# Kernel tuning notes

Measured on AMD Instinct MI355X. Metric: run time of the kernel, lower is better.

Reference implementation:

```python
import jax, jax.numpy as jnp
import numpy as np

NUM_SCALES = 3
LAMBDA_0 = 1.0
MU_0 = 1.0
KAPPA_LAMBDA = 0.5
KAPPA_MU = 0.5
BASE_WEIGHT = 1.0
GRADIENT_SCALING = 0.1


def tgradient(f, axis):
    """torch.gradient semantics: central diff interior, one-sided at edges (spacing=1)."""
    n = f.shape[axis]
    def sl(a, b):
        idx = [slice(None)] * f.ndim
        idx[axis] = slice(a, b)
        return f[tuple(idx)]
    interior = (sl(2, n) - sl(0, n - 2)) * 0.5
    first = sl(1, 2) - sl(0, 1)
    last = sl(n - 1, n) - sl(n - 2, n - 1)
    return jnp.concatenate([first, interior, last], axis=axis)


def resize1d_linear(x, axis, out_size):
    """1D linear resize along `axis` with align_corners=True."""
    in_size = x.shape[axis]
    if out_size == in_size:
        return x
    denom = max(out_size - 1, 1)
    coords = jnp.arange(out_size, dtype=jnp.float32) * ((in_size - 1) / denom)
    i0 = jnp.floor(coords).astype(jnp.int32)
    i1 = jnp.minimum(i0 + 1, in_size - 1)
    w = (coords - i0.astype(jnp.float32)).astype(x.dtype)
    shape = [1] * x.ndim
    shape[axis] = out_size
    w = w.reshape(shape)
    x0 = jnp.take(x, i0, axis=axis)
    x1 = jnp.take(x, i1, axis=axis)
    return x0 * (1 - w) + x1 * w


def trilinear_downsample(x, scale):
    # F.interpolate(..., scale_factor=1/scale, mode='trilinear', align_corners=True,
    # recompute_scale_factor=True): out_size = floor(in_size / scale); separable linear.
    for axis in (2, 3, 4):
        out_size = int(np.floor(x.shape[axis] / scale))
        x = resize1d_linear(x, axis, out_size)
    return x


def elasticity_loss(deformation_field, image):
    total_loss = jnp.float32(0.0)
    for i in range(NUM_SCALES):
        scale = 2 ** i
        deform = trilinear_downsample(deformation_field, scale)
        img = trilinear_downsample(image, scale)
        u, v, w = deform[:, 0], deform[:, 1], deform[:, 2]  # each (B, X, Y, Z)
        du_dx, du_dy, du_dz = tgradient(u, 1), tgradient(u, 2), tgradient(u, 3)
        dv_dx, dv_dy, dv_dz = tgradient(v, 1), tgradient(v, 2), tgradient(v, 3)
        dw_dx, dw_dy, dw_dz = tgradient(w, 1), tgradient(w, 2), tgradient(w, 3)
        E_xx, E_yy, E_zz = du_dx, dv_dy, dw_dz
        E_xy = 0.5 * (du_dy + dv_dx)
        E_xz = 0.5 * (du_dz + dw_dx)
        E_yz = 0.5 * (dv_dz + dw_dy)
        trace_E = E_xx + E_yy + E_zz
        ic = img[:, 0]  # (B, X, Y, Z)
        gx, gy, gz = tgradient(ic, 1), tgradient(ic, 2), tgradient(ic, 3)
        image_gradient = jnp.sqrt(gx * gx + gy * gy + gz * gz)
        adaptive_lambda = LAMBDA_0 + KAPPA_LAMBDA * image_gradient
        adaptive_mu = MU_0 + KAPPA_MU * image_gradient
        elastic_energy = (0.5 * adaptive_lambda * trace_E ** 2
                          + adaptive_mu * (E_xx ** 2 + E_yy ** 2 + E_zz ** 2
                                           + 2.0 * (E_xy ** 2 + E_xz ** 2 + E_yz ** 2)))
        adaptive_weight = BASE_WEIGHT + GRADIENT_SCALING * image_gradient
        total_loss = total_loss + jnp.mean(adaptive_weight * elastic_energy)
    return total_loss


def setup_inputs() -> dict:
    key = jax.random.key(0)
    k1, k2 = jax.random.split(key)
    deformation_field = jax.random.normal(k1, (2, 3, 160, 192, 160), dtype=jnp.float32)
    image = jax.random.uniform(k2, (2, 1, 160, 192, 160), dtype=jnp.float32)
    return {"deformation_field": deformation_field, "image": image}


def reference(deformation_field, image):
    return elasticity_loss(deformation_field, image)
```

## Files before the change

kernel.cpp:

```cpp
#include <hip/hip_runtime.h>
#include <math.h>


#define LAMBDA_0 1.0f
#define MU_0 1.0f
#define KAPPA_LAMBDA 0.5f
#define KAPPA_MU 0.5f
#define BASE_WEIGHT 1.0f
#define GRADIENT_SCALING 0.1f

constexpr int TY = 32;
constexpr int TZ = 32;
constexpr int CX = 10;
constexpr int PITCH = TZ + 4;
constexpr int ROWS = TY + 2;
constexpr int FSZ = ROWS * PITCH;

struct P4 {
    float4 a, b, c, d;
    float ha, hb, hc, hd;
};

__device__ __forceinline__ P4 loadPlane(const float* __restrict__ p0,
                                        const float* __restrict__ p1,
                                        const float* __restrict__ p2,
                                        const float* __restrict__ p3,
                                        long long po, long long ctrOff,
                                        bool hasHalo, long long haloOff) {
    P4 r;
    long long o = po + ctrOff;
    r.a = *(const float4*)(p0 + o);
    r.b = *(const float4*)(p1 + o);
    r.c = *(const float4*)(p2 + o);
    r.d = *(const float4*)(p3 + o);
    r.ha = r.hb = r.hc = r.hd = 0.f;
    if (hasHalo) {
        long long h = po + haloOff;
        r.ha = p0[h]; r.hb = p1[h]; r.hc = p2[h]; r.hd = p3[h];
    }
    return r;
}

__device__ __forceinline__ void storePlane(float* lds, const P4& pr,
                                           int ldsCtr, bool hasHalo, int hIdx) {
    *(float4*)(lds + 0 * FSZ + ldsCtr) = pr.a;
    *(float4*)(lds + 1 * FSZ + ldsCtr) = pr.b;
    *(float4*)(lds + 2 * FSZ + ldsCtr) = pr.c;
    *(float4*)(lds + 3 * FSZ + ldsCtr) = pr.d;
    if (hasHalo) {
        lds[0 * FSZ + hIdx] = pr.ha;
        lds[1 * FSZ + hIdx] = pr.hb;
        lds[2 * FSZ + hIdx] = pr.hc;
        lds[3 * FSZ + hIdx] = pr.hd;
    }
}

__device__ __forceinline__ void unpackC(const P4& p, float d[4][4]) {
    d[0][0] = p.a.x; d[0][1] = p.a.y; d[0][2] = p.a.z; d[0][3] = p.a.w;
    d[1][0] = p.b.x; d[1][1] = p.b.y; d[1][2] = p.b.z; d[1][3] = p.b.w;
    d[2][0] = p.c.x; d[2][1] = p.c.y; d[2][2] = p.c.z; d[2][3] = p.c.w;
    d[3][0] = p.d.x; d[3][1] = p.d.y; d[3][2] = p.d.z; d[3][3] = p.d.w;
}

__global__ void elasticity_stream_kernel(const float* __restrict__ def,
                                         const float* __restrict__ img,
                                         int X, int Y, int Z,
                                         int nby, int nbz, int nbx,
                                         float inv_n, float* __restrict__ out) {
    __shared__ __align__(16) float lds[4 * FSZ];

    int t = blockIdx.x;
    const int bx = t % nbx; t /= nbx;
    const int bz = t % nbz; t /= nbz;
    const int by = t % nby; t /= nby;
    const int b = t;

    const int tz = bz * TZ, ty = by * TY, x0 = bx * CX;
    const int tid = threadIdx.x;
    const int zg = tid & 7;
    const int ly = tid >> 3;

    const long long vol = (long long)X * Y * Z;
    const long long sX = (long long)Y * Z;
    const float* __restrict__ p0 = def + ((long long)b * 3 + 0) * vol;
    const float* __restrict__ p1 = def + ((long long)b * 3 + 1) * vol;
    const float* __restrict__ p2 = def + ((long long)b * 3 + 2) * vol;
    const float* __restrict__ p3 = img + (long long)b * vol;

    const int gy = ty + ly;
    const int gz0 = tz + 4 * zg;
    const long long ctrOff = (long long)gy * Z + gz0;
    const int ldsCtr = (ly + 1) * PITCH + 4 * zg;

    const bool hasHalo = (tid < 2 * (TZ + 2) + 2 * TY);
    int hIdx = 0;
    long long haloOff = 0;
    if (hasHalo) {
        int hr, hc;
        if (tid < TZ + 2)                { hr = 0;      hc = tid; }
        else if (tid < 2 * (TZ + 2))     { hr = TY + 1; hc = tid - (TZ + 2); }
        else if (tid < 2 * (TZ + 2) + TY){ hr = tid - 2 * (TZ + 2) + 1; hc = TZ; }
        else                             { hr = tid - (2 * (TZ + 2) + TY) + 1; hc = TZ + 1; }
        int zl = (hc < TZ) ? hc : ((hc == TZ) ? -1 : TZ);
        int hy = min(max(ty + hr - 1, 0), Y - 1);
        int hz = min(max(tz + zl, 0), Z - 1);
        haloOff = (long long)hy * Z + hz;
        hIdx = hr * PITCH + hc;
    }

    const bool ylo = (gy == 0), yhi = (gy == Y - 1);
    const bool zloE = (gz0 == 0), zhiE = (gz0 + 4 == Z);
    const int zmCol = (zg == 0) ? TZ : (4 * zg - 1);
    const int zpCol = (zg == 7) ? (TZ + 1) : (4 * zg + 4);
    const int rowM = ly * PITCH + 4 * zg;
    const int rowC = (ly + 1) * PITCH;
    const int rowP = (ly + 2) * PITCH + 4 * zg;

    float Cprev[4][4], Ccur[4][4], Cnext[4][4];
    {
        long long o = (long long)max(x0 - 1, 0) * sX + ctrOff;
        float4 a = *(const float4*)(p0 + o);
        float4 bq = *(const float4*)(p1 + o);
        float4 c = *(const float4*)(p2 + o);
        float4 d = *(const float4*)(p3 + o);
        Cprev[0][0]=a.x; Cprev[0][1]=a.y; Cprev[0][2]=a.z; Cprev[0][3]=a.w;
        Cprev[1][0]=bq.x;Cprev[1][1]=bq.y;Cprev[1][2]=bq.z;Cprev[1][3]=bq.w;
        Cprev[2][0]=c.x; Cprev[2][1]=c.y; Cprev[2][2]=c.z; Cprev[2][3]=c.w;
        Cprev[3][0]=d.x; Cprev[3][1]=d.y; Cprev[3][2]=d.z; Cprev[3][3]=d.w;
    }
    P4 cur = loadPlane(p0, p1, p2, p3, (long long)x0 * sX, ctrOff, hasHalo, haloOff);
    storePlane(lds, cur, ldsCtr, hasHalo, hIdx);
    unpackC(cur, Ccur);
    __syncthreads();
    P4 pn = loadPlane(p0, p1, p2, p3, (long long)(x0 + 1) * sX, ctrOff, hasHalo, haloOff);

    float acc = 0.f;
    for (int i = 0; i < CX; ++i) {
        const int x = x0 + i;
        const bool xlo = (x == 0), xhi = (x == X - 1);

        P4 q;
        const bool more = (i + 1 < CX);
        if (more) {
            long long xp = min(x + 2, X - 1);
            q = loadPlane(p0, p1, p2, p3, xp * sX, ctrOff, hasHalo, haloOff);
        }

        unpackC(pn, Cnext);

        float GX[4][4], GY[4][4], GZ[4][4];
#pragma unroll
        for (int f = 0; f < 4; ++f) {
            const float* L = lds + f * FSZ;
            float4 ym = *(const float4*)(L + rowM);
            float4 yp = *(const float4*)(L + rowP);
            float zm = L[rowC + zmCol];
            float zp = L[rowC + zpCol];
            float ymv[4] = {ym.x, ym.y, ym.z, ym.w};
            float ypv[4] = {yp.x, yp.y, yp.z, yp.w};
#pragma unroll
            for (int i2 = 0; i2 < 4; ++i2) {
                float C = Ccur[f][i2];
                GX[f][i2] = xlo ? (Cnext[f][i2] - C)
                                : (xhi ? (C - Cprev[f][i2])
                                       : 0.5f * (Cnext[f][i2] - Cprev[f][i2]));
                GY[f][i2] = ylo ? (ypv[i2] - C)
                                : (yhi ? (C - ymv[i2])
                                       : 0.5f * (ypv[i2] - ymv[i2]));
            }
            GZ[f][0] = zloE ? (Ccur[f][1] - Ccur[f][0]) : 0.5f * (Ccur[f][1] - zm);
            GZ[f][1] = 0.5f * (Ccur[f][2] - Ccur[f][0]);
            GZ[f][2] = 0.5f * (Ccur[f][3] - Ccur[f][1]);
            GZ[f][3] = zhiE ? (Ccur[f][3] - Ccur[f][2]) : 0.5f * (zp - Ccur[f][2]);
        }

#pragma unroll
        for (int i2 = 0; i2 < 4; ++i2) {
            float Exx = GX[0][i2], Eyy = GY[1][i2], Ezz = GZ[2][i2];
            float Exy = 0.5f * (GY[0][i2] + GX[1][i2]);
            float Exz = 0.5f * (GZ[0][i2] + GX[2][i2]);
            float Eyz = 0.5f * (GZ[1][i2] + GY[2][i2]);
            float tr = Exx + Eyy + Ezz;
            float g = sqrtf(GX[3][i2] * GX[3][i2] + GY[3][i2] * GY[3][i2] +
                            GZ[3][i2] * GZ[3][i2]);
            float lam = LAMBDA_0 + KAPPA_LAMBDA * g;
            float mu  = MU_0 + KAPPA_MU * g;
            float energy = 0.5f * lam * tr * tr +
                           mu * (Exx * Exx + Eyy * Eyy + Ezz * Ezz +
                                 2.0f * (Exy * Exy + Exz * Exz + Eyz * Eyz));
            float wgt = BASE_WEIGHT + GRADIENT_SCALING * g;
            acc += wgt * energy;
        }

        if (more) {
            __syncthreads();
            storePlane(lds, pn, ldsCtr, hasHalo, hIdx);
            __syncthreads();
#pragma unroll
            for (int f = 0; f < 4; ++f)
#pragma unroll
                for (int i2 = 0; i2 < 4; ++i2) {
                    Cprev[f][i2] = Ccur[f][i2];
                    Ccur[f][i2] = Cnext[f][i2];
                }
            pn = q;
        }
    }

    float val = acc * inv_n;
    for (int off = 32; off > 0; off >>= 1)
        val += __shfl_down(val, off, 64);
    __shared__ float smem[4];
    int wid = (int)(threadIdx.x >> 6);
    if ((threadIdx.x & 63) == 0) smem[wid] = val;
    __syncthreads();
    if (threadIdx.x == 0) {
        float s = smem[0] + smem[1] + smem[2] + smem[3];
        atomicAdd(out, s);
    }
}

__global__ void downsample_all8_kernel(const float* __restrict__ def,
                                       const float* __restrict__ img,
                                       float* __restrict__ odef,
                                       float* __restrict__ oimg,
                                       int inX, int inY, int inZ,
                                       int outX, int outY, int outZ,
                                       float rx, float ry, float rz) {
    long long pervol = (long long)outX * outY * outZ;
    long long total = 8LL * pervol;
    long long idx = (long long)blockIdx.x * blockDim.x + threadIdx.x;
    if (idx >= total) return;

    int m = (int)(idx / pervol);
    long long r = idx % pervol;
    int z = (int)(r % outZ);
    long long t = r / outZ;
    int y = (int)(t % outY);
    int x = (int)(t / outY);

    long long invol = (long long)inX * inY * inZ;
    const float* src;
    float* dst;
    if (m < 6) { src = def + (long long)m * invol;       dst = odef + (long long)m * pervol; }
    else       { src = img + (long long)(m - 6) * invol; dst = oimg + (long long)(m - 6) * pervol; }

    float cx = (float)x * rx;
    float cy = (float)y * ry;
    float cz = (float)z * rz;
    int ix0 = (int)floorf(cx), iy0 = (int)floorf(cy), iz0 = (int)floorf(cz);
    float wx = cx - (float)ix0, wy = cy - (float)iy0, wz = cz - (float)iz0;
    int ix1 = min(ix0 + 1, inX - 1);
    int iy1 = min(iy0 + 1, inY - 1);
    int iz1 = min(iz0 + 1, inZ - 1);

    long long sYZ = (long long)inY * inZ;
    long long bx0 = (long long)ix0 * sYZ, bx1 = (long long)ix1 * sYZ;
    long long by0 = (long long)iy0 * inZ, by1 = (long long)iy1 * inZ;

    float v000 = src[bx0 + by0 + iz0], v001 = src[bx0 + by0 + iz1];
    float v010 = src[bx0 + by1 + iz0], v011 = src[bx0 + by1 + iz1];
    float v100 = src[bx1 + by0 + iz0], v101 = src[bx1 + by0 + iz1];
    float v110 = src[bx1 + by1 + iz0], v111 = src[bx1 + by1 + iz1];

    float a00 = v000 * (1.f - wx) + v100 * wx;
    float a01 = v001 * (1.f - wx) + v101 * wx;
    float a10 = v010 * (1.f - wx) + v110 * wx;
    float a11 = v011 * (1.f - wx) + v111 * wx;
    float b0 = a00 * (1.f - wy) + a10 * wy;
    float b1 = a01 * (1.f - wy) + a11 * wy;
    dst[r] = b0 * (1.f - wz) + b1 * wz;
}

__global__ void elasticity_loss_v4_kernel(const float* __restrict__ def,
                                          const float* __restrict__ img,
                                          int B, int X, int Y, int Z,
                                          float inv_n,
                                          float* __restrict__ out) {
    const int Zg = Z >> 2;
    long long total = (long long)B * X * Y * Zg;
    long long idx = (long long)blockIdx.x * blockDim.x + threadIdx.x;
    float val = 0.f;
    if (idx < total) {
        int zg = (int)(idx % Zg);
        long long t = idx / Zg;
        int y = (int)(t % Y);
        t /= Y;
        int x = (int)(t % X);
        int b = (int)(t / X);
        int z0 = zg << 2;

        long long vol = (long long)X * Y * Z;
        const float* base0 = def + ((long long)b * 3 + 0) * vol;
        const float* base1 = def + ((long long)b * 3 + 1) * vol;
        const float* base2 = def + ((long long)b * 3 + 2) * vol;
        const float* base3 = img + (long long)b * vol;
        const float* bases[4] = {base0, base1, base2, base3};

        long long sX = (long long)Y * Z;
        long long c = (long long)x * sX + (long long)y * Z + z0;
        long long cxm = (x > 0) ? c - sX : c;
        long long cxp = (x < X - 1) ? c + sX : c;
        long long cym = (y > 0) ? c - Z : c;
        long long cyp = (y < Y - 1) ? c + Z : c;
        long long czm = (z0 > 0) ? c - 1 : c;
        long long czp = (z0 + 4 < Z) ? c + 4 : c;

        float C[4][4], XM[4][4], XP[4][4], YM[4][4], YP[4][4];
        float ZM[4], ZP[4];
#pragma unroll
        for (int f = 0; f < 4; ++f) {
            const float* p = bases[f];
            float4 tc = *(const float4*)(p + c);
            float4 txm = *(const float4*)(p + cxm);
            float4 txp = *(const float4*)(p + cxp);
            float4 tym = *(const float4*)(p + cym);
            float4 typ = *(const float4*)(p + cyp);
            ZM[f] = p[czm];
            ZP[f] = p[czp];
            C[f][0] = tc.x;  C[f][1] = tc.y;  C[f][2] = tc.z;  C[f][3] = tc.w;
            XM[f][0] = txm.x; XM[f][1] = txm.y; XM[f][2] = txm.z; XM[f][3] = txm.w;
            XP[f][0] = txp.x; XP[f][1] = txp.y; XP[f][2] = txp.z; XP[f][3] = txp.w;
            YM[f][0] = tym.x; YM[f][1] = tym.y; YM[f][2] = tym.z; YM[f][3] = tym.w;
            YP[f][0] = typ.x; YP[f][1] = typ.y; YP[f][2] = typ.z; YP[f][3] = typ.w;
        }

        const bool xlo = (x == 0), xhi = (x == X - 1);
        const bool ylo = (y == 0), yhi = (y == Y - 1);
        const bool zlo = (z0 == 0), zhi = (z0 + 4 == Z);

        float GX[4][4], GY[4][4], GZ[4][4];
#pragma unroll
        for (int f = 0; f < 4; ++f) {
#pragma unroll
            for (int i = 0; i < 4; ++i) {
                GX[f][i] = xlo ? (XP[f][i] - C[f][i])
                               : (xhi ? (C[f][i] - XM[f][i])
                                      : 0.5f * (XP[f][i] - XM[f][i]));
                GY[f][i] = ylo ? (YP[f][i] - C[f][i])
                               : (yhi ? (C[f][i] - YM[f][i])
                                      : 0.5f * (YP[f][i] - YM[f][i]));
            }
            GZ[f][0] = zlo ? (C[f][1] - C[f][0]) : 0.5f * (C[f][1] - ZM[f]);
            GZ[f][1] = 0.5f * (C[f][2] - C[f][0]);
            GZ[f][2] = 0.5f * (C[f][3] - C[f][1]);
            GZ[f][3] = zhi ? (C[f][3] - C[f][2]) : 0.5f * (ZP[f] - C[f][2]);
        }

        float acc = 0.f;
#pragma unroll
        for (int i = 0; i < 4; ++i) {
            float Exx = GX[0][i], Eyy = GY[1][i], Ezz = GZ[2][i];
            float Exy = 0.5f * (GY[0][i] + GX[1][i]);
            float Exz = 0.5f * (GZ[0][i] + GX[2][i]);
            float Eyz = 0.5f * (GZ[1][i] + GY[2][i]);
            float tr = Exx + Eyy + Ezz;
            float g = sqrtf(GX[3][i] * GX[3][i] + GY[3][i] * GY[3][i] +
                            GZ[3][i] * GZ[3][i]);
            float lam = LAMBDA_0 + KAPPA_LAMBDA * g;
            float mu  = MU_0 + KAPPA_MU * g;
            float energy = 0.5f * lam * tr * tr +
                           mu * (Exx * Exx + Eyy * Eyy + Ezz * Ezz +
                                 2.0f * (Exy * Exy + Exz * Exz + Eyz * Eyz));
            float wgt = BASE_WEIGHT + GRADIENT_SCALING * g;
            acc += wgt * energy;
        }
        val = acc * inv_n;
    }

    for (int off = 32; off > 0; off >>= 1)
        val += __shfl_down(val, off, 64);
    __shared__ float smem[8];
    int lane = threadIdx.x & 63;
    int wid = (int)(threadIdx.x >> 6);
    if (lane == 0) smem[wid] = val;
    __syncthreads();
    if (threadIdx.x == 0) {
        float s = 0.f;
        int nw = (int)(blockDim.x >> 6);
        for (int i = 0; i < nw; ++i) s += smem[i];
        atomicAdd(out, s);
    }
}

static void launch_loss_v4(const float* def, const float* img, int B, int X,
                           int Y, int Z, float* out, hipStream_t stream) {
    const int BLOCK = 256;
    long long nvox = (long long)B * X * Y * Z;
    long long total = nvox >> 2;
    float inv_n = (float)(1.0 / (double)nvox);
    int grid = (int)((total + BLOCK - 1) / BLOCK);
    elasticity_loss_v4_kernel<<<grid, BLOCK, 0, stream>>>(def, img, B, X, Y, Z,
                                                          inv_n, out);
}

extern "C" void kernel_launch(void* const* d_in, const int* in_sizes, int n_in,
                              void* d_out, int out_size, void* d_ws, size_t ws_size,
                              hipStream_t stream) {
    const float* def = (const float*)d_in[0];
    const float* img = (const float*)d_in[1];
    float* out = (float*)d_out;

    const int B = 2;
    const int X0 = 160, Y0 = 192, Z0 = 160;

    hipMemsetAsync(out, 0, sizeof(float), stream);

    const int BLOCK = 256;

    {
        long long nvox = (long long)B * X0 * Y0 * Z0;
        float inv_n = (float)(1.0 / (double)nvox);
        int nby = Y0 / TY;
        int nbz = Z0 / TZ;
        int nbx = X0 / CX;
        int grid = B * nby * nbz * nbx;
        elasticity_stream_kernel<<<grid, 256, 0, stream>>>(def, img, X0, Y0, Z0,
                                                           nby, nbz, nbx,
                                                           inv_n, out);
    }

    const int X2 = 80, Y2 = 96, Z2 = 80;
    const int X4 = 40, Y4 = 48, Z4 = 40;
    long long vol2 = (long long)X2 * Y2 * Z2;
    long long vol4 = (long long)X4 * Y4 * Z4;

    float* def2 = (float*)d_ws;
    float* img2 = def2 + (long long)B * 3 * vol2;
    float* def4 = img2 + (long long)B * vol2;
    float* img4 = def4 + (long long)B * 3 * vol4;

    {
        float rx = (float)((double)(X0 - 1) / (double)(X2 - 1));
        float ry = (float)((double)(Y0 - 1) / (double)(Y2 - 1));
        float rz = (float)((double)(Z0 - 1) / (double)(Z2 - 1));
        long long total = 8LL * vol2;
        int g = (int)((total + BLOCK - 1) / BLOCK);
        downsample_all8_kernel<<<g, BLOCK, 0, stream>>>(def, img, def2, img2,
                                                        X0, Y0, Z0, X2, Y2, Z2,
                                                        rx, ry, rz);
        launch_loss_v4(def2, img2, B, X2, Y2, Z2, out, stream);
    }

    {
        float rx = (float)((double)(X0 - 1) / (double)(X4 - 1));
        float ry = (float)((double)(Y0 - 1) / (double)(Y4 - 1));
        float rz = (float)((double)(Z0 - 1) / (double)(Z4 - 1));
        long long total = 8LL * vol4;
        int g = (int)((total + BLOCK - 1) / BLOCK);
        downsample_all8_kernel<<<g, BLOCK, 0, stream>>>(def, img, def4, img4,
                                                        X0, Y0, Z0, X4, Y4, Z4,
                                                        rx, ry, rz);
        launch_loss_v4(def4, img4, B, X4, Y4, Z4, out, stream);
    }
}
```

Measured before the change: 111.6 us.

## Double-buffer LDS planes and fetch z-neighbours via wavefront shuffles

The stencil kernel now keeps two LDS plane buffers, so the next x-plane is written into the spare buffer while the current one is being read. This replaces the two barriers per iteration with one. Interior z-neighbour values now come from lane shuffles of register data, and LDS is read only at the tile edges. The cost is twice the LDS footprint, which may lower occupancy, plus extra shuffle instructions.

New measurement: 114.2 us. 2.3% more time.

```diff
diff --git a/kernel.cpp b/kernel.cpp
--- a/kernel.cpp
+++ b/kernel.cpp
@@ -15,6 +15,7 @@
 constexpr int PITCH = TZ + 4;
 constexpr int ROWS = TY + 2;
 constexpr int FSZ = ROWS * PITCH;
+constexpr int BUFSZ = 4 * FSZ;
 
 struct P4 {
     float4 a, b, c, d;
@@ -41,17 +42,17 @@
     return r;
 }
 
-__device__ __forceinline__ void storePlane(float* lds, const P4& pr,
+__device__ __forceinline__ void storePlane(float* buf, const P4& pr,
                                            int ldsCtr, bool hasHalo, int hIdx) {
-    *(float4*)(lds + 0 * FSZ + ldsCtr) = pr.a;
-    *(float4*)(lds + 1 * FSZ + ldsCtr) = pr.b;
-    *(float4*)(lds + 2 * FSZ + ldsCtr) = pr.c;
-    *(float4*)(lds + 3 * FSZ + ldsCtr) = pr.d;
+    *(float4*)(buf + 0 * FSZ + ldsCtr) = pr.a;
+    *(float4*)(buf + 1 * FSZ + ldsCtr) = pr.b;
+    *(float4*)(buf + 2 * FSZ + ldsCtr) = pr.c;
+    *(float4*)(buf + 3 * FSZ + ldsCtr) = pr.d;
     if (hasHalo) {
-        lds[0 * FSZ + hIdx] = pr.ha;
-        lds[1 * FSZ + hIdx] = pr.hb;
-        lds[2 * FSZ + hIdx] = pr.hc;
-        lds[3 * FSZ + hIdx] = pr.hd;
+        buf[0 * FSZ + hIdx] = pr.ha;
+        buf[1 * FSZ + hIdx] = pr.hb;
+        buf[2 * FSZ + hIdx] = pr.hc;
+        buf[3 * FSZ + hIdx] = pr.hd;
     }
 }
 
@@ -62,12 +63,13 @@
     d[3][0] = p.d.x; d[3][1] = p.d.y; d[3][2] = p.d.z; d[3][3] = p.d.w;
 }
 
-__global__ void elasticity_stream_kernel(const float* __restrict__ def,
-                                         const float* __restrict__ img,
-                                         int X, int Y, int Z,
-                                         int nby, int nbz, int nbx,
-                                         float inv_n, float* __restrict__ out) {
-    __shared__ __align__(16) float lds[4 * FSZ];
+__global__ void elasticity_stream_db_kernel(const float* __restrict__ def,
+                                            const float* __restrict__ img,
+                                            int X, int Y, int Z,
+                                            int nby, int nbz, int nbx,
+                                            float inv_n,
+                                            float* __restrict__ out) {
+    __shared__ __align__(16) float lds[2 * BUFSZ];
 
     int t = blockIdx.x;
     const int bx = t % nbx; t /= nbx;
@@ -79,6 +81,9 @@
     const int tid = threadIdx.x;
     const int zg = tid & 7;
     const int ly = tid >> 3;
+    const int lane = tid & 63;
+    const int laneM = (lane - 1) & 63;
+    const int laneP = (lane + 1) & 63;
 
     const long long vol = (long long)X * Y * Z;
     const long long sX = (long long)Y * Z;
@@ -110,8 +115,7 @@
 
     const bool ylo = (gy == 0), yhi = (gy == Y - 1);
     const bool zloE = (gz0 == 0), zhiE = (gz0 + 4 == Z);
-    const int zmCol = (zg == 0) ? TZ : (4 * zg - 1);
-    const int zpCol = (zg == 7) ? (TZ + 1) : (4 * zg + 4);
+    const bool zem = (zg == 0), zep = (zg == 7);
     const int rowM = ly * PITCH + 4 * zg;
     const int rowC = (ly + 1) * PITCH;
     const int rowP = (ly + 2) * PITCH + 4 * zg;
@@ -131,31 +135,36 @@
     P4 cur = loadPlane(p0, p1, p2, p3, (long long)x0 * sX, ctrOff, hasHalo, haloOff);
     storePlane(lds, cur, ldsCtr, hasHalo, hIdx);
     unpackC(cur, Ccur);
+    P4 pn = loadPlane(p0, p1, p2, p3, (long long)(x0 + 1) * sX, ctrOff, hasHalo, haloOff);
     __syncthreads();
-    P4 pn = loadPlane(p0, p1, p2, p3, (long long)(x0 + 1) * sX, ctrOff, hasHalo, haloOff);
 
     float acc = 0.f;
     for (int i = 0; i < CX; ++i) {
         const int x = x0 + i;
         const bool xlo = (x == 0), xhi = (x == X - 1);
+        const bool more = (i + 1 < CX);
+        float* ldsCur = lds + (i & 1) * BUFSZ;
+        float* ldsNxt = lds + ((i + 1) & 1) * BUFSZ;
 
         P4 q;
-        const bool more = (i + 1 < CX);
         if (more) {
             long long xp = min(x + 2, X - 1);
             q = loadPlane(p0, p1, p2, p3, xp * sX, ctrOff, hasHalo, haloOff);
         }
 
         unpackC(pn, Cnext);
+        if (more) storePlane(ldsNxt, pn, ldsCtr, hasHalo, hIdx);
 
         float GX[4][4], GY[4][4], GZ[4][4];
 #pragma unroll
         for (int f = 0; f < 4; ++f) {
-            const float* L = lds + f * FSZ;
+            const float* L = ldsCur + f * FSZ;
             float4 ym = *(const float4*)(L + rowM);
             float4 yp = *(const float4*)(L + rowP);
-            float zm = L[rowC + zmCol];
-            float zp = L[rowC + zpCol];
+            float zmv = __shfl(Ccur[f][3], laneM, 64);
+            float zpv = __shfl(Ccur[f][0], laneP, 64);
+            float zm = zem ? L[rowC + TZ]     : zmv;
+            float zp = zep ? L[rowC + TZ + 1] : zpv;
             float ymv[4] = {ym.x, ym.y, ym.z, ym.w};
             float ypv[4] = {yp.x, yp.y, yp.z, yp.w};
 #pragma unroll
@@ -193,9 +202,6 @@
         }
 
         if (more) {
-            __syncthreads();
-            storePlane(lds, pn, ldsCtr, hasHalo, hIdx);
-            __syncthreads();
 #pragma unroll
             for (int f = 0; f < 4; ++f)
 #pragma unroll
@@ -204,6 +210,7 @@
                     Ccur[f][i2] = Cnext[f][i2];
                 }
             pn = q;
+            __syncthreads();
         }
     }
 
@@ -415,9 +422,10 @@
         int nbz = Z0 / TZ;
         int nbx = X0 / CX;
         int grid = B * nby * nbz * nbx;
-        elasticity_stream_kernel<<<grid, 256, 0, stream>>>(def, img, X0, Y0, Z0,
-                                                           nby, nbz, nbx,
-                                                           inv_n, out);
+        elasticity_stream_db_kernel<<<grid, 256, 0, stream>>>(def, img,
+                                                              X0, Y0, Z0,
+                                                              nby, nbz, nbx,
+                                                              inv_n, out);
     }
 
     const int X2 = 80, Y2 = 96, Z2 = 80;
```

## Merge full-res stream and downsample kernels, fuse coarse-scale loss kernels

Applied to the files above, without the earlier changes.

Cuts the launch count from five kernels to two. The full-resolution streaming stencil and both trilinear downsamples now share one grid, with extra blocks doing the downsampling. The loss kernels for the two coarser scales are merged into a single launch that picks its scale from the block index. This removes launch overhead and lets the downsample blocks overlap with the streaming blocks, but mixes heterogeneous blocks whose LDS footprint and register pressure follow the larger stream path.

Result: slower. 142.0 us (+27.2%).

```diff
diff --git a/kernel.cpp b/kernel.cpp
--- a/kernel.cpp
+++ b/kernel.cpp
@@ -15,6 +15,20 @@
 constexpr int PITCH = TZ + 4;
 constexpr int ROWS = TY + 2;
 constexpr int FSZ = ROWS * PITCH;
+
+constexpr int BATCH = 2;
+constexpr int X0 = 160, Y0 = 192, Z0 = 160;
+constexpr int X2 = 80, Y2 = 96, Z2 = 80;
+constexpr int X4 = 40, Y4 = 48, Z4 = 40;
+constexpr long long VOL2 = (long long)X2 * Y2 * Z2;
+constexpr long long VOL4 = (long long)X4 * Y4 * Z4;
+
+constexpr int NBY = Y0 / TY;
+constexpr int NBZ = Z0 / TZ;
+constexpr int NBX = X0 / CX;
+constexpr int N_STREAM = BATCH * NBY * NBZ * NBX;
+constexpr int N_DS2 = (int)(8 * VOL2 / 256);
+constexpr int N_DS4 = (int)(8 * VOL4 / 256);
 
 struct P4 {
     float4 a, b, c, d;
@@ -62,17 +76,86 @@
     d[3][0] = p.d.x; d[3][1] = p.d.y; d[3][2] = p.d.z; d[3][3] = p.d.w;
 }
 
-__global__ void elasticity_stream_kernel(const float* __restrict__ def,
-                                         const float* __restrict__ img,
-                                         int X, int Y, int Z,
-                                         int nby, int nbz, int nbx,
-                                         float inv_n, float* __restrict__ out) {
+__device__ __forceinline__ void ds_body(const float* __restrict__ def,
+                                        const float* __restrict__ img,
+                                        float* __restrict__ odef,
+                                        float* __restrict__ oimg,
+                                        int inX, int inY, int inZ,
+                                        int outX, int outY, int outZ,
+                                        float rx, float ry, float rz,
+                                        long long idx) {
+    long long pervol = (long long)outX * outY * outZ;
+    int m = (int)(idx / pervol);
+    long long r = idx % pervol;
+    int z = (int)(r % outZ);
+    long long t = r / outZ;
+    int y = (int)(t % outY);
+    int x = (int)(t / outY);
+
+    long long invol = (long long)inX * inY * inZ;
+    const float* src;
+    float* dst;
+    if (m < 6) { src = def + (long long)m * invol;       dst = odef + (long long)m * pervol; }
+    else       { src = img + (long long)(m - 6) * invol; dst = oimg + (long long)(m - 6) * pervol; }
+
+    float cx = (float)x * rx;
+    float cy = (float)y * ry;
+    float cz = (float)z * rz;
+    int ix0 = (int)floorf(cx), iy0 = (int)floorf(cy), iz0 = (int)floorf(cz);
+    float wx = cx - (float)ix0, wy = cy - (float)iy0, wz = cz - (float)iz0;
+    int ix1 = min(ix0 + 1, inX - 1);
+    int iy1 = min(iy0 + 1, inY - 1);
+    int iz1 = min(iz0 + 1, inZ - 1);
+
+    long long sYZ = (long long)inY * inZ;
+    long long bx0 = (long long)ix0 * sYZ, bx1 = (long long)ix1 * sYZ;
+    long long by0 = (long long)iy0 * inZ, by1 = (long long)iy1 * inZ;
+
+    float v000 = src[bx0 + by0 + iz0], v001 = src[bx0 + by0 + iz1];
+    float v010 = src[bx0 + by1 + iz0], v011 = src[bx0 + by1 + iz1];
+    float v100 = src[bx1 + by0 + iz0], v101 = src[bx1 + by0 + iz1];
+    float v110 = src[bx1 + by1 + iz0], v111 = src[bx1 + by1 + iz1];
+
+    float a00 = v000 * (1.f - wx) + v100 * wx;
+    float a01 = v001 * (1.f - wx) + v101 * wx;
+    float a10 = v010 * (1.f - wx) + v110 * wx;
+    float a11 = v011 * (1.f - wx) + v111 * wx;
+    float b0 = a00 * (1.f - wy) + a10 * wy;
+    float b1 = a01 * (1.f - wy) + a11 * wy;
+    dst[r] = b0 * (1.f - wz) + b1 * wz;
+}
+
+__global__ void mega_stream_ds_kernel(const float* __restrict__ def,
+                                      const float* __restrict__ img,
+                                      float* __restrict__ def2,
+                                      float* __restrict__ img2,
+                                      float* __restrict__ def4,
+                                      float* __restrict__ img4,
+                                      float rx2, float ry2, float rz2,
+                                      float rx4, float ry4, float rz4,
+                                      float inv_n0,
+                                      float* __restrict__ out) {
     __shared__ __align__(16) float lds[4 * FSZ];
 
+    if (blockIdx.x >= N_STREAM) {
+        int db = blockIdx.x - N_STREAM;
+        if (db < N_DS2) {
+            long long idx = (long long)db * 256 + threadIdx.x;
+            ds_body(def, img, def2, img2, X0, Y0, Z0, X2, Y2, Z2,
+                    rx2, ry2, rz2, idx);
+        } else {
+            long long idx = (long long)(db - N_DS2) * 256 + threadIdx.x;
+            ds_body(def, img, def4, img4, X0, Y0, Z0, X4, Y4, Z4,
+                    rx4, ry4, rz4, idx);
+        }
+        return;
+    }
+
+    const int X = X0, Y = Y0, Z = Z0;
     int t = blockIdx.x;
-    const int bx = t % nbx; t /= nbx;
-    const int bz = t % nbz; t /= nbz;
-    const int by = t % nby; t /= nby;
+    const int bx = t % NBX; t /= NBX;
+    const int bz = t % NBZ; t /= NBZ;
+    const int by = t % NBY; t /= NBY;
     const int b = t;
 
     const int tz = bz * TZ, ty = by * TY, x0 = bx * CX;
@@ -207,7 +290,7 @@
         }
     }
 
-    float val = acc * inv_n;
+    float val = acc * inv_n0;
     for (int off = 32; off > 0; off >>= 1)
         val += __shfl_down(val, off, 64);
     __shared__ float smem[4];
@@ -215,183 +298,129 @@
     if ((threadIdx.x & 63) == 0) smem[wid] = val;
     __syncthreads();
     if (threadIdx.x == 0) {
-        float s = smem[0] + smem[1] + smem[2] + smem[3];
-        atomicAdd(out, s);
-    }
-}
-
-__global__ void downsample_all8_kernel(const float* __restrict__ def,
-                                       const float* __restrict__ img,
-                                       float* __restrict__ odef,
-                                       float* __restrict__ oimg,
-                                       int inX, int inY, int inZ,
-                                       int outX, int outY, int outZ,
-                                       float rx, float ry, float rz) {
-    long long pervol = (long long)outX * outY * outZ;
-    long long total = 8LL * pervol;
-    long long idx = (long long)blockIdx.x * blockDim.x + threadIdx.x;
-    if (idx >= total) return;
-
-    int m = (int)(idx / pervol);
-    long long r = idx % pervol;
-    int z = (int)(r % outZ);
-    long long t = r / outZ;
-    int y = (int)(t % outY);
-    int x = (int)(t / outY);
-
-    long long invol = (long long)inX * inY * inZ;
-    const float* src;
-    float* dst;
-    if (m < 6) { src = def + (long long)m * invol;       dst = odef + (long long)m * pervol; }
-    else       { src = img + (long long)(m - 6) * invol; dst = oimg + (long long)(m - 6) * pervol; }
-
-    float cx = (float)x * rx;
-    float cy = (float)y * ry;
-    float cz = (float)z * rz;
-    int ix0 = (int)floorf(cx), iy0 = (int)floorf(cy), iz0 = (int)floorf(cz);
-    float wx = cx - (float)ix0, wy = cy - (float)iy0, wz = cz - (float)iz0;
-    int ix1 = min(ix0 + 1, inX - 1);
-    int iy1 = min(iy0 + 1, inY - 1);
-    int iz1 = min(iz0 + 1, inZ - 1);
-
-    long long sYZ = (long long)inY * inZ;
-    long long bx0 = (long long)ix0 * sYZ, bx1 = (long long)ix1 * sYZ;
-    long long by0 = (long long)iy0 * inZ, by1 = (long long)iy1 * inZ;
-
-    float v000 = src[bx0 + by0 + iz0], v001 = src[bx0 + by0 + iz1];
-    float v010 = src[bx0 + by1 + iz0], v011 = src[bx0 + by1 + iz1];
-    float v100 = src[bx1 + by0 + iz0], v101 = src[bx1 + by0 + iz1];
-    float v110 = src[bx1 + by1 + iz0], v111 = src[bx1 + by1 + iz1];
-
-    float a00 = v000 * (1.f - wx) + v100 * wx;
-    float a01 = v001 * (1.f - wx) + v101 * wx;
-    float a10 = v010 * (1.f - wx) + v110 * wx;
-    float a11 = v011 * (1.f - wx) + v111 * wx;
-    float b0 = a00 * (1.f - wy) + a10 * wy;
-    float b1 = a01 * (1.f - wy) + a11 * wy;
-    dst[r] = b0 * (1.f - wz) + b1 * wz;
-}
-
-__global__ void elasticity_loss_v4_kernel(const float* __restrict__ def,
-                                          const float* __restrict__ img,
-                                          int B, int X, int Y, int Z,
-                                          float inv_n,
-                                          float* __restrict__ out) {
+        atomicAdd(out, smem[0] + smem[1] + smem[2] + smem[3]);
+    }
+}
+
+__device__ __forceinline__ float loss_body(const float* __restrict__ def,
+                                           const float* __restrict__ img,
+                                           int B, int X, int Y, int Z,
+                                           long long idx) {
     const int Zg = Z >> 2;
-    long long total = (long long)B * X * Y * Zg;
-    long long idx = (long long)blockIdx.x * blockDim.x + threadIdx.x;
-    float val = 0.f;
-    if (idx < total) {
-        int zg = (int)(idx % Zg);
-        long long t = idx / Zg;
-        int y = (int)(t % Y);
-        t /= Y;
-        int x = (int)(t % X);
-        int b = (int)(t / X);
-        int z0 = zg << 2;
-
-        long long vol = (long long)X * Y * Z;
-        const float* base0 = def + ((long long)b * 3 + 0) * vol;
-        const float* base1 = def + ((long long)b * 3 + 1) * vol;
-        const float* base2 = def + ((long long)b * 3 + 2) * vol;
-        const float* base3 = img + (long long)b * vol;
-        const float* bases[4] = {base0, base1, base2, base3};
-
-        long long sX = (long long)Y * Z;
-        long long c = (long long)x * sX + (long long)y * Z + z0;
-        long long cxm = (x > 0) ? c - sX : c;
-        long long cxp = (x < X - 1) ? c + sX : c;
-        long long cym = (y > 0) ? c - Z : c;
-        long long cyp = (y < Y - 1) ? c + Z : c;
-        long long czm = (z0 > 0) ? c - 1 : c;
-        long long czp = (z0 + 4 < Z) ? c + 4 : c;
-
-        float C[4][4], XM[4][4], XP[4][4], YM[4][4], YP[4][4];
-        float ZM[4], ZP[4];
-#pragma unroll
-        for (int f = 0; f < 4; ++f) {
-            const float* p = bases[f];
-            float4 tc = *(const float4*)(p + c);
-            float4 txm = *(const float4*)(p + cxm);
-            float4 txp = *(const float4*)(p + cxp);
-            float4 tym = *(const float4*)(p + cym);
-            float4 typ = *(const float4*)(p + cyp);
-            ZM[f] = p[czm];
-            ZP[f] = p[czp];
-            C[f][0] = tc.x;  C[f][1] = tc.y;  C[f][2] = tc.z;  C[f][3] = tc.w;
-            XM[f][0] = txm.x; XM[f][1] = txm.y; XM[f][2] = txm.z; XM[f][3] = txm.w;
-            XP[f][0] = txp.x; XP[f][1] = txp.y; XP[f][2] = txp.z; XP[f][3] = txp.w;
-            YM[f][0] = tym.x; YM[f][1] = tym.y; YM[f][2] = tym.z; YM[f][3] = tym.w;
-            YP[f][0] = typ.x; YP[f][1] = typ.y; YP[f][2] = typ.z; YP[f][3] = typ.w;
-        }
-
-        const bool xlo = (x == 0), xhi = (x == X - 1);
-        const bool ylo = (y == 0), yhi = (y == Y - 1);
-        const bool zlo = (z0 == 0), zhi = (z0 + 4 == Z);
-
-        float GX[4][4], GY[4][4], GZ[4][4];
-#pragma unroll
-        for (int f = 0; f < 4; ++f) {
-#pragma unroll
-            for (int i = 0; i < 4; ++i) {
-                GX[f][i] = xlo ? (XP[f][i] - C[f][i])
-                               : (xhi ? (C[f][i] - XM[f][i])
-                                      : 0.5f * (XP[f][i] - XM[f][i]));
-                GY[f][i] = ylo ? (YP[f][i] - C[f][i])
-                               : (yhi ? (C[f][i] - YM[f][i])
-                                      : 0.5f * (YP[f][i] - YM[f][i]));
-            }
-            GZ[f][0] = zlo ? (C[f][1] - C[f][0]) : 0.5f * (C[f][1] - ZM[f]);
-            GZ[f][1] = 0.5f * (C[f][2] - C[f][0]);
-            GZ[f][2] = 0.5f * (C[f][3] - C[f][1]);
-            GZ[f][3] = zhi ? (C[f][3] - C[f][2]) : 0.5f * (ZP[f] - C[f][2]);
-        }
-
-        float acc = 0.f;
+    int zg = (int)(idx % Zg);
+    long long t = idx / Zg;
+    int y = (int)(t % Y);
+    t /= Y;
+    int x = (int)(t % X);
+    int b = (int)(t / X);
+    (void)B;
+    int z0 = zg << 2;
+
+    long long vol = (long long)X * Y * Z;
+    const float* base0 = def + ((long long)b * 3 + 0) * vol;
+    const float* base1 = def + ((long long)b * 3 + 1) * vol;
+    const float* base2 = def + ((long long)b * 3 + 2) * vol;
+    const float* base3 = img + (long long)b * vol;
+    const float* bases[4] = {base0, base1, base2, base3};
+
+    long long sX = (long long)Y * Z;
+    long long c = (long long)x * sX + (long long)y * Z + z0;
+    long long cxm = (x > 0) ? c - sX : c;
+    long long cxp = (x < X - 1) ? c + sX : c;
+    long long cym = (y > 0) ? c - Z : c;
+    long long cyp = (y < Y - 1) ? c + Z : c;
+    long long czm = (z0 > 0) ? c - 1 : c;
+    long long czp = (z0 + 4 < Z) ? c + 4 : c;
+
+    float C[4][4], XM[4][4], XP[4][4], YM[4][4], YP[4][4];
+    float ZM[4], ZP[4];
+#pragma unroll
+    for (int f = 0; f < 4; ++f) {
+        const float* p = bases[f];
+        float4 tc = *(const float4*)(p + c);
+        float4 txm = *(const float4*)(p + cxm);
+        float4 txp = *(const float4*)(p + cxp);
+        float4 tym = *(const float4*)(p + cym);
+        float4 typ = *(const float4*)(p + cyp);
+        ZM[f] = p[czm];
+        ZP[f] = p[czp];
+        C[f][0] = tc.x;  C[f][1] = tc.y;  C[f][2] = tc.z;  C[f][3] = tc.w;
+        XM[f][0] = txm.x; XM[f][1] = txm.y; XM[f][2] = txm.z; XM[f][3] = txm.w;
+        XP[f][0] = txp.x; XP[f][1] = txp.y; XP[f][2] = txp.z; XP[f][3] = txp.w;
+        YM[f][0] = tym.x; YM[f][1] = tym.y; YM[f][2] = tym.z; YM[f][3] = tym.w;
+        YP[f][0] = typ.x; YP[f][1] = typ.y; YP[f][2] = typ.z; YP[f][3] = typ.w;
+    }
+
+    const bool xlo = (x == 0), xhi = (x == X - 1);
+    const bool ylo = (y == 0), yhi = (y == Y - 1);
+    const bool zlo = (z0 == 0), zhi = (z0 + 4 == Z);
+
+    float GX[4][4], GY[4][4], GZ[4][4];
+#pragma unroll
+    for (int f = 0; f < 4; ++f) {
 #pragma unroll
         for (int i = 0; i < 4; ++i) {
-            float Exx = GX[0][i], Eyy = GY[1][i], Ezz = GZ[2][i];
-            float Exy = 0.5f * (GY[0][i] + GX[1][i]);
-            float Exz = 0.5f * (GZ[0][i] + GX[2][i]);
-            float Eyz = 0.5f * (GZ[1][i] + GY[2][i]);
-            float tr = Exx + Eyy + Ezz;
-            float g = sqrtf(GX[3][i] * GX[3][i] + GY[3][i] * GY[3][i] +
-                            GZ[3][i] * GZ[3][i]);
-            float lam = LAMBDA_0 + KAPPA_LAMBDA * g;
-            float mu  = MU_0 + KAPPA_MU * g;
-            float energy = 0.5f * lam * tr * tr +
-                           mu * (Exx * Exx + Eyy * Eyy + Ezz * Ezz +
-                                 2.0f * (Exy * Exy + Exz * Exz + Eyz * Eyz));
-            float wgt = BASE_WEIGHT + GRADIENT_SCALING * g;
-            acc += wgt * energy;
-        }
-        val = acc * inv_n;
+            GX[f][i] = xlo ? (XP[f][i] - C[f][i])
+                           : (xhi ? (C[f][i] - XM[f][i])
+                                  : 0.5f * (XP[f][i] - XM[f][i]));
+            GY[f][i] = ylo ? (YP[f][i] - C[f][i])
+                           : (yhi ? (C[f][i] - YM[f][i])
+                                  : 0.5f * (YP[f][i] - YM[f][i]));
+        }
+        GZ[f][0] = zlo ? (C[f][1] - C[f][0]) : 0.5f * (C[f][1] - ZM[f]);
+        GZ[f][1] = 0.5f * (C[f][2] - C[f][0]);
+        GZ[f][2] = 0.5f * (C[f][3] - C[f][1]);
+        GZ[f][3] = zhi ? (C[f][3] - C[f][2]) : 0.5f * (ZP[f] - C[f][2]);
+    }
+
+    float acc = 0.f;
+#pragma unroll
+    for (int i = 0; i < 4; ++i) {
+        float Exx = GX[0][i], Eyy = GY[1][i], Ezz = GZ[2][i];
+        float Exy = 0.5f * (GY[0][i] + GX[1][i]);
+        float Exz = 0.5f * (GZ[0][i] + GX[2][i]);
+        float Eyz = 0.5f * (GZ[1][i] + GY[2][i]);
+        float tr = Exx + Eyy + Ezz;
+        float g = sqrtf(GX[3][i] * GX[3][i] + GY[3][i] * GY[3][i] +
+                        GZ[3][i] * GZ[3][i]);
+        float lam = LAMBDA_0 + KAPPA_LAMBDA * g;
+        float mu  = MU_0 + KAPPA_MU * g;
+        float energy = 0.5f * lam * tr * tr +
+                       mu * (Exx * Exx + Eyy * Eyy + Ezz * Ezz +
+                             2.0f * (Exy * Exy + Exz * Exz + Eyz * Eyz));
+        float wgt = BASE_WEIGHT + GRADIENT_SCALING * g;
+        acc += wgt * energy;
+    }
+    return acc;
+}
+
+constexpr int G_LOSS2 = (int)(BATCH * VOL2 / 4 / 256);
+constexpr int G_LOSS4 = (int)(BATCH * VOL4 / 4 / 256);
+
+__global__ void fused_loss_kernel(const float* __restrict__ def2,
+                                  const float* __restrict__ img2,
+                                  const float* __restrict__ def4,
+                                  const float* __restrict__ img4,
+                                  float inv_n2, float inv_n4,
+                                  float* __restrict__ out) {
+    float val;
+    if (blockIdx.x < G_LOSS2) {
+        long long idx = (long long)blockIdx.x * 256 + threadIdx.x;
+        val = loss_body(def2, img2, BATCH, X2, Y2, Z2, idx) * inv_n2;
+    } else {
+        long long idx = (long long)(blockIdx.x - G_LOSS2) * 256 + threadIdx.x;
+        val = loss_body(def4, img4, BATCH, X4, Y4, Z4, idx) * inv_n4;
     }
 
     for (int off = 32; off > 0; off >>= 1)
         val += __shfl_down(val, off, 64);
-    __shared__ float smem[8];
-    int lane = threadIdx.x & 63;
+    __shared__ float smem[4];
     int wid = (int)(threadIdx.x >> 6);
-    if (lane == 0) smem[wid] = val;
+    if ((threadIdx.x & 63) == 0) smem[wid] = val;
     __syncthreads();
     if (threadIdx.x == 0) {
-        float s = 0.f;
-        int nw = (int)(blockDim.x >> 6);
-        for (int i = 0; i < nw; ++i) s += smem[i];
-        atomicAdd(out, s);
-    }
-}
-
-static void launch_loss_v4(const float* def, const float* img, int B, int X,
-                           int Y, int Z, float* out, hipStream_t stream) {
-    const int BLOCK = 256;
-    long long nvox = (long long)B * X * Y * Z;
-    long long total = nvox >> 2;
-    float inv_n = (float)(1.0 / (double)nvox);
-    int grid = (int)((total + BLOCK - 1) / BLOCK);
-    elasticity_loss_v4_kernel<<<grid, BLOCK, 0, stream>>>(def, img, B, X, Y, Z,
-                                                          inv_n, out);
+        atomicAdd(out, smem[0] + smem[1] + smem[2] + smem[3]);
+    }
 }
 
 extern "C" void kernel_launch(void* const* d_in, const int* in_sizes, int n_in,
@@ -401,56 +430,36 @@
     const float* img = (const float*)d_in[1];
     float* out = (float*)d_out;
 
-    const int B = 2;
-    const int X0 = 160, Y0 = 192, Z0 = 160;
-
-    hipMemsetAsync(out, 0, sizeof(float), stream);
-
-    const int BLOCK = 256;
+    (void)hipMemsetAsync(out, 0, sizeof(float), stream);
+
+    float* def2 = (float*)d_ws;
+    float* img2 = def2 + (long long)BATCH * 3 * VOL2;
+    float* def4 = img2 + (long long)BATCH * VOL2;
+    float* img4 = def4 + (long long)BATCH * 3 * VOL4;
+
+    const float rx2 = (float)((double)(X0 - 1) / (double)(X2 - 1));
+    const float ry2 = (float)((double)(Y0 - 1) / (double)(Y2 - 1));
+    const float rz2 = (float)((double)(Z0 - 1) / (double)(Z2 - 1));
+    const float rx4 = (float)((double)(X0 - 1) / (double)(X4 - 1));
+    const float ry4 = (float)((double)(Y0 - 1) / (double)(Y4 - 1));
+    const float rz4 = (float)((double)(Z0 - 1) / (double)(Z4 - 1));
+
+    const float inv_n0 = (float)(1.0 / (double)((long long)BATCH * X0 * Y0 * Z0));
+    const float inv_n2 = (float)(1.0 / (double)(BATCH * VOL2));
+    const float inv_n4 = (float)(1.0 / (double)(BATCH * VOL4));
 
     {
-        long long nvox = (long long)B * X0 * Y0 * Z0;
-        float inv_n = (float)(1.0 / (double)nvox);
-        int nby = Y0 / TY;
-        int nbz = Z0 / TZ;
-        int nbx = X0 / CX;
-        int grid = B * nby * nbz * nbx;
-        elasticity_stream_kernel<<<grid, 256, 0, stream>>>(def, img, X0, Y0, Z0,
-                                                           nby, nbz, nbx,
-                                                           inv_n, out);
-    }
-
-    const int X2 = 80, Y2 = 96, Z2 = 80;
-    const int X4 = 40, Y4 = 48, Z4 = 40;
-    long long vol2 = (long long)X2 * Y2 * Z2;
-    long long vol4 = (long long)X4 * Y4 * Z4;
-
-    float* def2 = (float*)d_ws;
-    float* img2 = def2 + (long long)B * 3 * vol2;
-    float* def4 = img2 + (long long)B * vol2;
-    float* img4 = def4 + (long long)B * 3 * vol4;
+        int grid = N_STREAM + N_DS2 + N_DS4;
+        mega_stream_ds_kernel<<<grid, 256, 0, stream>>>(def, img,
+                                                        def2, img2, def4, img4,
+                                                        rx2, ry2, rz2,
+                                                        rx4, ry4, rz4,
+                                                        inv_n0, out);
+    }
 
     {
-        float rx = (float)((double)(X0 - 1) / (double)(X2 - 1));
-        float ry = (float)((double)(Y0 - 1) / (double)(Y2 - 1));
-        float rz = (float)((double)(Z0 - 1) / (double)(Z2 - 1));
-        long long total = 8LL * vol2;
-        int g = (int)((total + BLOCK - 1) / BLOCK);
-        downsample_all8_kernel<<<g, BLOCK, 0, stream>>>(def, img, def2, img2,
-                                                        X0, Y0, Z0, X2, Y2, Z2,
-                                                        rx, ry, rz);
-        launch_loss_v4(def2, img2, B, X2, Y2, Z2, out, stream);
-    }
-
-    {
-        float rx = (float)((double)(X0 - 1) / (double)(X4 - 1));
-        float ry = (float)((double)(Y0 - 1) / (double)(Y4 - 1));
-        float rz = (float)((double)(Z0 - 1) / (double)(Z4 - 1));
-        long long total = 8LL * vol4;
-        int g = (int)((total + BLOCK - 1) / BLOCK);
-        downsample_all8_kernel<<<g, BLOCK, 0, stream>>>(def, img, def4, img4,
-                                                        X0, Y0, Z0, X4, Y4, Z4,
-                                                        rx, ry, rz);
-        launch_loss_v4(def4, img4, B, X4, Y4, Z4, out, stream);
-    }
-}
+        int grid = G_LOSS2 + G_LOSS4;
+        fused_loss_kernel<<<grid, 256, 0, stream>>>(def2, img2, def4, img4,
+                                                    inv_n2, inv_n4, out);
+    }
+}
```
